# Optimization experiments

Hardware: AMD Instinct MI355X
Metric: run time of the kernel (lower is better)

The kernel has to match this reference:

```python
import jax, jax.numpy as jnp
import numpy as np

BN_EPS = 1e-5

def _mlp(h, w1, b1, w2, b2):
    return jax.nn.relu(h @ w1 + b1) @ w2 + b2

def _segment_mean(data, seg, num_segments):
    s = jax.ops.segment_sum(data, seg, num_segments=num_segments)
    c = jax.ops.segment_sum(jnp.ones((data.shape[0],), data.dtype), seg, num_segments=num_segments)
    return s / jnp.maximum(c, 1.0)[:, None]

def _lin_init(k, fan_in, fan_out):
    k1, k2 = jax.random.split(k)
    s = 1.0 / float(np.sqrt(fan_in))
    w = jax.random.uniform(k1, (fan_in, fan_out), jnp.float32, -s, s)
    b = jax.random.uniform(k2, (fan_out,), jnp.float32, -s, s)
    return w, b

def setup_inputs() -> dict:
    key = jax.random.key(0)
    ks = jax.random.split(key, 16)
    N, E, B = 100000, 1600000, 256
    d1, d2, d3, d5, nc = 3, 50, 15, 10, 6
    x = jax.random.normal(ks[0], (N, d1), jnp.float32)
    edge_index = jax.random.randint(ks[1], (2, E), 0, N)
    edge_attr = jax.random.normal(ks[2], (E, d1), jnp.float32)
    u = jax.random.normal(ks[3], (B, 1), jnp.float32)
    batch = jnp.sort(jax.random.randint(ks[4], (N,), 0, B))
    ew1, eb1 = _lin_init(ks[5], d1 * 3, d2)
    ew2, eb2 = _lin_init(ks[6], d2, d3)
    nw1, nb1 = _lin_init(ks[7], d1 * 6, d2)
    nw2, nb2 = _lin_init(ks[8], d2, d3)
    gw1, gb1 = _lin_init(ks[9], d3 + 1, d2)
    gw2, gb2 = _lin_init(ks[10], d2, d3)
    fc1_w, fc1_b = _lin_init(ks[11], d3, d5)
    bn_g = jnp.ones((d5,), jnp.float32)
    bn_b = jnp.zeros((d5,), jnp.float32)
    fc2_w, fc2_b = _lin_init(ks[12], d5, nc)
    return dict(x=x, edge_index=edge_index, edge_attr=edge_attr, u=u, batch=batch,
                ew1=ew1, eb1=eb1, ew2=ew2, eb2=eb2,
                nw1=nw1, nb1=nb1, nw2=nw2, nb2=nb2,
                gw1=gw1, gb1=gb1, gw2=gw2, gb2=gb2,
                fc1_w=fc1_w, fc1_b=fc1_b, bn_g=bn_g, bn_b=bn_b,
                fc2_w=fc2_w, fc2_b=fc2_b)

def reference(x, edge_index, edge_attr, u, batch,
              ew1, eb1, ew2, eb2, nw1, nb1, nw2, nb2,
              gw1, gb1, gw2, gb2, fc1_w, fc1_b, bn_g, bn_b, fc2_w, fc2_b):
    N = x.shape[0]
    B = u.shape[0]
    row, col = edge_index[0], edge_index[1]
    # edge update: cat([x[row], x[col], edge_attr]) -> MLP  => [E, d3]
    e2 = _mlp(jnp.concatenate([x[row], x[col], edge_attr], axis=1), ew1, eb1, ew2, eb2)
    # node update: cat([x[col], e2]) -> MLP -> scatter_mean over row  => [N, d3]
    h = _mlp(jnp.concatenate([x[col], e2], axis=1), nw1, nb1, nw2, nb2)
    x2 = _segment_mean(h, row, N)
    # global update: cat([u, mean_per_graph(x2)]) -> MLP  => [B, d3]
    u2 = _mlp(jnp.concatenate([u, _segment_mean(x2, batch, B)], axis=1), gw1, gb1, gw2, gb2)
    # readout: relu(cat nodes + globals), mean-pool per graph (u2 rows join their graph)
    z = jax.nn.relu(jnp.concatenate([x2, u2], axis=0))  # dropout off (eval mode)
    seg = jnp.concatenate([batch, jnp.arange(B, dtype=batch.dtype)])
    g = _segment_mean(z, seg, B)  # [B, d3]
    h1 = g @ fc1_w + fc1_b
    # BatchNorm1d in eval mode with default running stats (mean=0, var=1)
    h1 = jax.nn.relu(h1 * (bn_g / jnp.sqrt(1.0 + BN_EPS)) + bn_b)
    return jax.nn.log_softmax(h1 @ fc2_w + fc2_b, axis=1)
```

## Files before the change

### kernel.cpp

```cpp
#include <hip/hip_runtime.h>
#include <math.h>

#define D1 3
#define D2 50
#define D3 15
#define D5 10
#define NC 6
#define SCAN_B 512

typedef _Float16 h2 __attribute__((ext_vector_type(2)));
typedef __fp16   fp16x2 __attribute__((ext_vector_type(2)));

__device__ __forceinline__ float fdot2(h2 a, h2 b, float c) {
#if __has_builtin(__builtin_amdgcn_fdot2)
    return __builtin_amdgcn_fdot2(a, b, c, false);
#else
    return c + (float)a[0] * (float)b[0] + (float)a[1] * (float)b[1];
#endif
}

__device__ __forceinline__ h2 pkrtz(float a, float b) {
#if __has_builtin(__builtin_amdgcn_cvt_pkrtz)
    fp16x2 r = __builtin_amdgcn_cvt_pkrtz(a, b);
    return __builtin_bit_cast(h2, r);
#else
    h2 v; v[0] = (_Float16)a; v[1] = (_Float16)b; return v;
#endif
}

__global__ __launch_bounds__(256) void deg_rank_prep_kernel(
    const int* __restrict__ ei, int* __restrict__ deg, int* __restrict__ rank, int E,
    const float* __restrict__ ew1, const float* __restrict__ nw1,
    const float* __restrict__ ew2, const float* __restrict__ nw2,
    h2* __restrict__ ew1pk, h2* __restrict__ nw1pk,
    h2* __restrict__ ew2pk, h2* __restrict__ nw2pk)
{
    int e = blockIdx.x * blockDim.x + threadIdx.x;
    if (e < E) {
        int r = ei[e];
        rank[e] = atomicAdd(&deg[r], 1);
    }
    if (blockIdx.x == 0) {
        int t = threadIdx.x;
        for (int i = t; i < D2 * 5; i += 256) {
            int j = i / 5, p = i - 5 * j;
            float a = ew1[(2 * p) * D2 + j];
            float b = (2 * p + 1 < 9) ? ew1[(2 * p + 1) * D2 + j] : 0.0f;
            h2 v; v[0] = (_Float16)a; v[1] = (_Float16)b;
            ew1pk[i] = v;
        }
        for (int i = t; i < D2 * 9; i += 256) {
            int j = i / 9, p = i - 9 * j;
            float a = nw1[(2 * p) * D2 + j];
            float b = nw1[(2 * p + 1) * D2 + j];
            h2 v; v[0] = (_Float16)a; v[1] = (_Float16)b;
            nw1pk[i] = v;
        }
        for (int i = t; i < D3 * 25; i += 256) {
            int m = i / 25, k = i - 25 * m;
            float a = ew2[(2 * k) * D3 + m];
            float b = ew2[(2 * k + 1) * D3 + m];
            h2 v; v[0] = (_Float16)a; v[1] = (_Float16)b;
            ew2pk[i] = v;
            float c = nw2[(2 * k) * D3 + m];
            float d = nw2[(2 * k + 1) * D3 + m];
            h2 w; w[0] = (_Float16)c; w[1] = (_Float16)d;
            nw2pk[i] = w;
        }
    }
}

__global__ __launch_bounds__(SCAN_B) void scan1_kernel(
    const int* __restrict__ deg, int* __restrict__ base, int* __restrict__ bsum, int N)
{
    __shared__ int sm[SCAN_B];
    int i = blockIdx.x * SCAN_B + threadIdx.x;
    int v = (i < N) ? deg[i] : 0;
    sm[threadIdx.x] = v;
    __syncthreads();
    #pragma unroll
    for (int s = 1; s < SCAN_B; s <<= 1) {
        int t = (threadIdx.x >= (unsigned)s) ? sm[threadIdx.x - s] : 0;
        __syncthreads();
        sm[threadIdx.x] += t;
        __syncthreads();
    }
    if (i < N) base[i] = sm[threadIdx.x] - v;
    if (threadIdx.x == SCAN_B - 1) bsum[blockIdx.x] = sm[threadIdx.x];
}

__global__ __launch_bounds__(1024) void scan2_kernel(int* __restrict__ bsum, int nb)
{
    __shared__ int sm[1024];
    int v = ((int)threadIdx.x < nb) ? bsum[threadIdx.x] : 0;
    sm[threadIdx.x] = v;
    __syncthreads();
    #pragma unroll
    for (int s = 1; s < 1024; s <<= 1) {
        int t = (threadIdx.x >= (unsigned)s) ? sm[threadIdx.x - s] : 0;
        __syncthreads();
        sm[threadIdx.x] += t;
        __syncthreads();
    }
    if ((int)threadIdx.x < nb) bsum[threadIdx.x] = sm[threadIdx.x] - v;
}

__global__ __launch_bounds__(SCAN_B) void scan3_kernel(
    int* __restrict__ base, const int* __restrict__ bsum, int N)
{
    int i = blockIdx.x * SCAN_B + threadIdx.x;
    if (i < N) base[i] += bsum[blockIdx.x];
}

__global__ __launch_bounds__(256, 4) void edge_mlp_fused_kernel(
    const float* __restrict__ x,
    const int*   __restrict__ ei,
    const float* __restrict__ ea,
    const h2* __restrict__ ew1pk, const float* __restrict__ eb1,
    const h2* __restrict__ ew2pk, const float* __restrict__ eb2,
    const h2* __restrict__ nw1pk, const float* __restrict__ nb1,
    const h2* __restrict__ nw2pk, const float* __restrict__ nb2,
    const int* __restrict__ base, const int* __restrict__ rank,
    unsigned int* __restrict__ hbuf16,
    int E)
{
    int e = blockIdx.x * blockDim.x + threadIdx.x;
    if (e >= E) return;

    int r = ei[e];
    int c = ei[E + e];
    int slot = base[r] + rank[e];

    float in9[9];
    in9[0] = x[3 * r + 0];
    in9[1] = x[3 * r + 1];
    in9[2] = x[3 * r + 2];
    in9[3] = x[3 * c + 0];
    in9[4] = x[3 * c + 1];
    in9[5] = x[3 * c + 2];
    in9[6] = ea[3 * e + 0];
    in9[7] = ea[3 * e + 1];
    in9[8] = ea[3 * e + 2];

    h2 inpk[5];
    inpk[0] = pkrtz(in9[0], in9[1]);
    inpk[1] = pkrtz(in9[2], in9[3]);
    inpk[2] = pkrtz(in9[4], in9[5]);
    inpk[3] = pkrtz(in9[6], in9[7]);
    inpk[4] = pkrtz(in9[8], 0.0f);

    h2 hpk[25];
    #pragma unroll
    for (int jj = 0; jj < 25; ++jj) {
        float a0 = eb1[2 * jj];
        float a1 = eb1[2 * jj + 1];
        #pragma unroll
        for (int p = 0; p < 5; ++p) {
            a0 = fdot2(inpk[p], ew1pk[(2 * jj) * 5 + p], a0);
            a1 = fdot2(inpk[p], ew1pk[(2 * jj + 1) * 5 + p], a1);
        }
        hpk[jj] = pkrtz(fmaxf(a0, 0.0f), fmaxf(a1, 0.0f));
    }

    float e2v[D3];
    #pragma unroll
    for (int m = 0; m < D3; ++m) {
        float a = eb2[m];
        #pragma unroll
        for (int k = 0; k < 25; ++k) a = fdot2(hpk[k], ew2pk[m * 25 + k], a);
        e2v[m] = a;
    }

    h2 vpk[9];
    vpk[0] = pkrtz(in9[3], in9[4]);
    vpk[1] = pkrtz(in9[5], e2v[0]);
    #pragma unroll
    for (int p = 2; p < 9; ++p) vpk[p] = pkrtz(e2v[2 * p - 3], e2v[2 * p - 2]);

    h2 h2pk[25];
    #pragma unroll
    for (int jj = 0; jj < 25; ++jj) {
        float a0 = nb1[2 * jj];
        float a1 = nb1[2 * jj + 1];
        #pragma unroll
        for (int p = 0; p < 9; ++p) {
            a0 = fdot2(vpk[p], nw1pk[(2 * jj) * 9 + p], a0);
            a1 = fdot2(vpk[p], nw1pk[(2 * jj + 1) * 9 + p], a1);
        }
        h2pk[jj] = pkrtz(fmaxf(a0, 0.0f), fmaxf(a1, 0.0f));
    }

    float acc[D3 + 1];
    #pragma unroll
    for (int m = 0; m < D3; ++m) {
        float a = nb2[m];
        #pragma unroll
        for (int k = 0; k < 25; ++k) a = fdot2(h2pk[k], nw2pk[m * 25 + k], a);
        acc[m] = a;
    }
    acc[D3] = 0.0f;

    union { h2 h[8]; uint4 u[2]; } outp;
    #pragma unroll
    for (int p = 0; p < 8; ++p) outp.h[p] = pkrtz(acc[2 * p], acc[2 * p + 1]);

    uint4* dst = (uint4*)(hbuf16 + (size_t)slot * 8);
    dst[0] = outp.u[0];
    dst[1] = outp.u[1];
}

__global__ __launch_bounds__(256) void tail_kernel(
    const unsigned int* __restrict__ hbuf16,
    const int* __restrict__ deg, const int* __restrict__ base,
    const int* __restrict__ batch, int N,
    const float* __restrict__ u,
    const float* __restrict__ gw1, const float* __restrict__ gb1,
    const float* __restrict__ gw2, const float* __restrict__ gb2,
    const float* __restrict__ fc1w, const float* __restrict__ fc1b,
    const float* __restrict__ bng, const float* __restrict__ bnb,
    const float* __restrict__ fc2w, const float* __restrict__ fc2b,
    float* __restrict__ out)
{
    int b = blockIdx.x;
    int tid = threadIdx.x;

    int lo = 0, hi = N;
    while (lo < hi) { int m = (lo + hi) >> 1; if (batch[m] < b) lo = m + 1; else hi = m; }
    int start = lo;
    hi = N;
    while (lo < hi) { int m = (lo + hi) >> 1; if (batch[m] < b + 1) lo = m + 1; else hi = m; }
    int end = lo;

    float sx[D3], sr[D3];
    #pragma unroll
    for (int j = 0; j < D3; ++j) { sx[j] = 0.0f; sr[j] = 0.0f; }

    for (int i = start + tid; i < end; i += 256) {
        int bs = deg ? base[i] : 0;
        int d  = deg[i];
        float acc[16];
        #pragma unroll
        for (int j = 0; j < 16; ++j) acc[j] = 0.0f;
        const uint4* ptr = (const uint4*)(hbuf16 + (size_t)bs * 8);
        for (int k = 0; k < d; ++k) {
            uint4 w0 = ptr[2 * k];
            uint4 w1 = ptr[2 * k + 1];
            unsigned int ws[8] = {w0.x, w0.y, w0.z, w0.w, w1.x, w1.y, w1.z, w1.w};
            #pragma unroll
            for (int p = 0; p < 8; ++p) {
                h2 v = __builtin_bit_cast(h2, ws[p]);
                acc[2 * p]     += (float)v[0];
                acc[2 * p + 1] += (float)v[1];
            }
        }
        float inv = 1.0f / fmaxf((float)d, 1.0f);
        #pragma unroll
        for (int j = 0; j < D3; ++j) {
            float v = acc[j] * inv;
            sx[j] += v;
            sr[j] += fmaxf(v, 0.0f);
        }
    }

    #pragma unroll
    for (int j = 0; j < D3; ++j) {
        #pragma unroll
        for (int s = 32; s > 0; s >>= 1) {
            sx[j] += __shfl_down(sx[j], s);
            sr[j] += __shfl_down(sr[j], s);
        }
    }

    __shared__ float sm[4][2 * D3];
    __shared__ float s_red[2 * D3];
    __shared__ float s_in16[16];
    __shared__ float s_gh[D2];
    __shared__ float s_g[D3];
    __shared__ float s_h1[D5];

    int lane = tid & 63, wid = tid >> 6;
    if (lane == 0) {
        #pragma unroll
        for (int j = 0; j < D3; ++j) { sm[wid][j] = sx[j]; sm[wid][D3 + j] = sr[j]; }
    }
    __syncthreads();

    float nct = (float)(end - start);

    if (tid < 2 * D3) {
        s_red[tid] = sm[0][tid] + sm[1][tid] + sm[2][tid] + sm[3][tid];
    }
    __syncthreads();

    if (tid < 16) {
        s_in16[tid] = (tid == 0) ? u[b] : s_red[tid - 1] / fmaxf(nct, 1.0f);
    }
    __syncthreads();

    if (tid < D2) {
        float a = gb1[tid];
        #pragma unroll
        for (int k = 0; k < 16; ++k) a = fmaf(s_in16[k], gw1[k * D2 + tid], a);
        s_gh[tid] = fmaxf(a, 0.0f);
    }
    __syncthreads();

    if (tid < D3) {
        float a = gb2[tid];
        #pragma unroll
        for (int k = 0; k < D2; ++k) a = fmaf(s_gh[k], gw2[k * D3 + tid], a);
        s_g[tid] = (s_red[D3 + tid] + fmaxf(a, 0.0f)) / (nct + 1.0f);
    }
    __syncthreads();

    if (tid < D5) {
        const float bnscale = 1.0f / sqrtf(1.0f + 1e-5f);
        float a = fc1b[tid];
        #pragma unroll
        for (int k = 0; k < D3; ++k) a = fmaf(s_g[k], fc1w[k * D5 + tid], a);
        s_h1[tid] = fmaxf(a * (bng[tid] * bnscale) + bnb[tid], 0.0f);
    }
    __syncthreads();

    if (tid == 0) {
        float o[NC];
        #pragma unroll
        for (int j = 0; j < NC; ++j) {
            float a = fc2b[j];
            #pragma unroll
            for (int k = 0; k < D5; ++k) a = fmaf(s_h1[k], fc2w[k * NC + j], a);
            o[j] = a;
        }
        float m = o[0];
        #pragma unroll
        for (int j = 1; j < NC; ++j) m = fmaxf(m, o[j]);
        float ssum = 0.0f;
        #pragma unroll
        for (int j = 0; j < NC; ++j) ssum += expf(o[j] - m);
        float lse = m + logf(ssum);
        #pragma unroll
        for (int j = 0; j < NC; ++j) out[b * NC + j] = o[j] - lse;
    }
}

__global__ __launch_bounds__(256) void edge_node_atomic_kernel(
    const float* __restrict__ x,
    const int*   __restrict__ ei,
    const float* __restrict__ ea,
    const float* __restrict__ ew1, const float* __restrict__ eb1,
    const float* __restrict__ ew2, const float* __restrict__ eb2,
    const float* __restrict__ nw1, const float* __restrict__ nb1,
    const float* __restrict__ nw2, const float* __restrict__ nb2,
    float* __restrict__ x2sum, float* __restrict__ cnt,
    int E)
{
    int e = blockIdx.x * blockDim.x + threadIdx.x;
    if (e >= E) return;
    int r = ei[e];
    int c = ei[E + e];
    float in9[9];
    in9[0] = x[3 * r + 0]; in9[1] = x[3 * r + 1]; in9[2] = x[3 * r + 2];
    float xc0 = x[3 * c + 0], xc1 = x[3 * c + 1], xc2 = x[3 * c + 2];
    in9[3] = xc0; in9[4] = xc1; in9[5] = xc2;
    in9[6] = ea[3 * e + 0]; in9[7] = ea[3 * e + 1]; in9[8] = ea[3 * e + 2];
    float h[D2];
    #pragma unroll
    for (int j = 0; j < D2; ++j) {
        float a = eb1[j];
        #pragma unroll
        for (int k = 0; k < 9; ++k) a = fmaf(in9[k], ew1[k * D2 + j], a);
        h[j] = fmaxf(a, 0.0f);
    }
    float e2[D3];
    #pragma unroll
    for (int j = 0; j < D3; ++j) {
        float a = eb2[j];
        #pragma unroll
        for (int k = 0; k < D2; ++k) a = fmaf(h[k], ew2[k * D3 + j], a);
        e2[j] = a;
    }
    float h2v[D2];
    #pragma unroll
    for (int j = 0; j < D2; ++j) {
        float a = nb1[j];
        a = fmaf(xc0, nw1[0 * D2 + j], a);
        a = fmaf(xc1, nw1[1 * D2 + j], a);
        a = fmaf(xc2, nw1[2 * D2 + j], a);
        #pragma unroll
        for (int k = 0; k < D3; ++k) a = fmaf(e2[k], nw1[(3 + k) * D2 + j], a);
        h2v[j] = fmaxf(a, 0.0f);
    }
    float* dst = x2sum + (size_t)r * D3;
    #pragma unroll
    for (int j = 0; j < D3; ++j) {
        float a = nb2[j];
        #pragma unroll
        for (int k = 0; k < D2; ++k) a = fmaf(h2v[k], nw2[k * D3 + j], a);
        atomicAdd(&dst[j], a);
    }
    atomicAdd(&cnt[r], 1.0f);
}

__global__ __launch_bounds__(256) void graph_sum_atomic_kernel(
    const float* __restrict__ x2sum, const float* __restrict__ cnt,
    const int* __restrict__ batch, int N,
    float* __restrict__ bx, float* __restrict__ brelu, float* __restrict__ ncnt)
{
    int b = blockIdx.x;
    int lo = 0, hi = N;
    while (lo < hi) { int m = (lo + hi) >> 1; if (batch[m] < b) lo = m + 1; else hi = m; }
    int start = lo;
    hi = N;
    while (lo < hi) { int m = (lo + hi) >> 1; if (batch[m] < b + 1) lo = m + 1; else hi = m; }
    int end = lo;
    float sx[D3], sr[D3];
    #pragma unroll
    for (int j = 0; j < D3; ++j) { sx[j] = 0.0f; sr[j] = 0.0f; }
    for (int i = start + (int)threadIdx.x; i < end; i += (int)blockDim.x) {
        float inv = 1.0f / fmaxf(cnt[i], 1.0f);
        #pragma unroll
        for (int j = 0; j < D3; ++j) {
            float v = x2sum[(size_t)i * D3 + j] * inv;
            sx[j] += v;
            sr[j] += fmaxf(v, 0.0f);
        }
    }
    #pragma unroll
    for (int j = 0; j < D3; ++j) {
        #pragma unroll
        for (int s = 32; s > 0; s >>= 1) {
            sx[j] += __shfl_down(sx[j], s);
            sr[j] += __shfl_down(sr[j], s);
        }
    }
    __shared__ float sm[4][2 * D3];
    int lane = threadIdx.x & 63, wid = threadIdx.x >> 6;
    if (lane == 0) {
        #pragma unroll
        for (int j = 0; j < D3; ++j) { sm[wid][j] = sx[j]; sm[wid][D3 + j] = sr[j]; }
    }
    __syncthreads();
    if (threadIdx.x < 2 * D3) {
        float v = sm[0][threadIdx.x] + sm[1][threadIdx.x] + sm[2][threadIdx.x] + sm[3][threadIdx.x];
        if (threadIdx.x < D3) bx[b * D3 + threadIdx.x] = v;
        else                  brelu[b * D3 + (threadIdx.x - D3)] = v;
    }
    if (threadIdx.x == 0) ncnt[b] = (float)(end - start);
}

__global__ __launch_bounds__(256) void final_kernel(
    const float* __restrict__ u,
    const float* __restrict__ gw1, const float* __restrict__ gb1,
    const float* __restrict__ gw2, const float* __restrict__ gb2,
    const float* __restrict__ fc1w, const float* __restrict__ fc1b,
    const float* __restrict__ bng, const float* __restrict__ bnb,
    const float* __restrict__ fc2w, const float* __restrict__ fc2b,
    const float* __restrict__ bx, const float* __restrict__ brelu,
    const float* __restrict__ ncnt,
    float* __restrict__ out, int B)
{
    int t = blockIdx.x * blockDim.x + threadIdx.x;
    if (t >= B) return;

    float nct = ncnt[t];
    float inv = 1.0f / fmaxf(nct, 1.0f);

    float in16[16];
    in16[0] = u[t];
    #pragma unroll
    for (int j = 0; j < D3; ++j) in16[1 + j] = bx[t * D3 + j] * inv;

    float gh[D2];
    #pragma unroll
    for (int j = 0; j < D2; ++j) {
        float a = gb1[j];
        #pragma unroll
        for (int k = 0; k < 16; ++k) a = fmaf(in16[k], gw1[k * D2 + j], a);
        gh[j] = fmaxf(a, 0.0f);
    }

    float g[D3];
    #pragma unroll
    for (int j = 0; j < D3; ++j) {
        float a = gb2[j];
        #pragma unroll
        for (int k = 0; k < D2; ++k) a = fmaf(gh[k], gw2[k * D3 + j], a);
        g[j] = (brelu[t * D3 + j] + fmaxf(a, 0.0f)) / (nct + 1.0f);
    }

    const float bnscale = 1.0f / sqrtf(1.0f + 1e-5f);
    float h1[D5];
    #pragma unroll
    for (int i = 0; i < D5; ++i) {
        float a = fc1b[i];
        #pragma unroll
        for (int k = 0; k < D3; ++k) a = fmaf(g[k], fc1w[k * D5 + i], a);
        h1[i] = fmaxf(a * (bng[i] * bnscale) + bnb[i], 0.0f);
    }

    float o[NC];
    #pragma unroll
    for (int j = 0; j < NC; ++j) {
        float a = fc2b[j];
        #pragma unroll
        for (int k = 0; k < D5; ++k) a = fmaf(h1[k], fc2w[k * NC + j], a);
        o[j] = a;
    }
    float m = o[0];
    #pragma unroll
    for (int j = 1; j < NC; ++j) m = fmaxf(m, o[j]);
    float ssum = 0.0f;
    #pragma unroll
    for (int j = 0; j < NC; ++j) ssum += expf(o[j] - m);
    float lse = m + logf(ssum);
    #pragma unroll
    for (int j = 0; j < NC; ++j) out[t * NC + j] = o[j] - lse;
}

extern "C" void kernel_launch(void* const* d_in, const int* in_sizes, int n_in,
                              void* d_out, int out_size, void* d_ws, size_t ws_size,
                              hipStream_t stream) {
    const float* x     = (const float*)d_in[0];
    const int*   ei    = (const int*)  d_in[1];
    const float* ea    = (const float*)d_in[2];
    const float* u     = (const float*)d_in[3];
    const int*   batch = (const int*)  d_in[4];
    const float* ew1 = (const float*)d_in[5];
    const float* eb1 = (const float*)d_in[6];
    const float* ew2 = (const float*)d_in[7];
    const float* eb2 = (const float*)d_in[8];
    const float* nw1 = (const float*)d_in[9];
    const float* nb1 = (const float*)d_in[10];
    const float* nw2 = (const float*)d_in[11];
    const float* nb2 = (const float*)d_in[12];
    const float* gw1 = (const float*)d_in[13];
    const float* gb1 = (const float*)d_in[14];
    const float* gw2 = (const float*)d_in[15];
    const float* gb2 = (const float*)d_in[16];
    const float* fc1w = (const float*)d_in[17];
    const float* fc1b = (const float*)d_in[18];
    const float* bng  = (const float*)d_in[19];
    const float* bnb  = (const float*)d_in[20];
    const float* fc2w = (const float*)d_in[21];
    const float* fc2b = (const float*)d_in[22];

    int N = in_sizes[0] / 3;
    int E = in_sizes[2] / 3;
    int B = in_sizes[3];
    float* out = (float*)d_out;

    int nsb = (N + SCAN_B - 1) / SCAN_B;

    const size_t WPK = 2048;

    size_t need = sizeof(h2) * WPK
                + sizeof(unsigned int) * (size_t)E * 8
                + sizeof(int) * ((size_t)N + (size_t)E + (size_t)N + 1024);

    if (ws_size >= need && nsb <= 1024) {
        char* p = (char*)d_ws;
        h2* ew1pk = (h2*)p;
        h2* nw1pk = ew1pk + 250;
        h2* ew2pk = nw1pk + 450;
        h2* nw2pk = ew2pk + 375;
        p += sizeof(h2) * WPK;
        unsigned int* hbuf16 = (unsigned int*)p;  p += sizeof(unsigned int) * (size_t)E * 8;
        int* deg  = (int*)p;            p += sizeof(int) * (size_t)N;
        int* rank = (int*)p;            p += sizeof(int) * (size_t)E;
        int* base = (int*)p;            p += sizeof(int) * (size_t)N;
        int* bsum = (int*)p;            p += sizeof(int) * 1024;

        hipMemsetAsync(deg, 0, sizeof(int) * (size_t)N, stream);

        int eb = (E + 255) / 256;
        deg_rank_prep_kernel<<<eb, 256, 0, stream>>>(
            ei, deg, rank, E, ew1, nw1, ew2, nw2, ew1pk, nw1pk, ew2pk, nw2pk);

        scan1_kernel<<<nsb, SCAN_B, 0, stream>>>(deg, base, bsum, N);
        scan2_kernel<<<1, 1024, 0, stream>>>(bsum, nsb);
        scan3_kernel<<<nsb, SCAN_B, 0, stream>>>(base, bsum, N);

        edge_mlp_fused_kernel<<<eb, 256, 0, stream>>>(
            x, ei, ea, ew1pk, eb1, ew2pk, eb2, nw1pk, nb1, nw2pk, nb2,
            base, rank, hbuf16, E);

        tail_kernel<<<B, 256, 0, stream>>>(
            hbuf16, deg, base, batch, N,
            u, gw1, gb1, gw2, gb2, fc1w, fc1b, bng, bnb, fc2w, fc2b, out);
    } else {
        float* x2sum = (float*)d_ws;
        float* cnt   = x2sum + (size_t)N * D3;
        float* bx    = cnt + N;
        float* brelu = bx + (size_t)B * D3;
        float* ncnt  = brelu + (size_t)B * D3;

        hipMemsetAsync(x2sum, 0, sizeof(float) * ((size_t)N * D3 + N), stream);

        int eb = (E + 255) / 256;
        edge_node_atomic_kernel<<<eb, 256, 0, stream>>>(
            x, ei, ea, ew1, eb1, ew2, eb2, nw1, nb1, nw2, nb2, x2sum, cnt, E);

        graph_sum_atomic_kernel<<<B, 256, 0, stream>>>(x2sum, cnt, batch, N, bx, brelu, ncnt);

        int fb = (B + 255) / 256;
        final_kernel<<<fb, 256, 0, stream>>>(
            u, gw1, gb1, gw2, gb2, fc1w, fc1b, bng, bnb, fc2w, fc2b,
            bx, brelu, ncnt, out, B);
    }
}
```

Baseline: 209.5 us.

## Parallelize tail reduction across nodes and merge scan passes

Replaces the per-graph tail kernel (256 blocks, one per graph) with a node-parallel partial kernel. Eight threads per node each sum one fp16 pair of that node's segment, then atomically add into shared-memory per-graph accumulators that are flushed to a global gsum buffer. A separate single-thread-per-graph head kernel then runs the small MLP and log-softmax. The second and third scan passes are also fused into one kernel in which each block sums the preceding block totals itself. This targets the low parallelism of the old tail, at the cost of more atomics and redundant bsum reads.

```diff
diff --git a/kernel.cpp b/kernel.cpp
--- a/kernel.cpp
+++ b/kernel.cpp
@@ -7,6 +7,7 @@
 #define D5 10
 #define NC 6
 #define SCAN_B 512
+#define GS 64
 
 typedef _Float16 h2 __attribute__((ext_vector_type(2)));
 typedef __fp16   fp16x2 __attribute__((ext_vector_type(2)));
@@ -89,27 +90,28 @@
     if (threadIdx.x == SCAN_B - 1) bsum[blockIdx.x] = sm[threadIdx.x];
 }
 
-__global__ __launch_bounds__(1024) void scan2_kernel(int* __restrict__ bsum, int nb)
-{
-    __shared__ int sm[1024];
-    int v = ((int)threadIdx.x < nb) ? bsum[threadIdx.x] : 0;
-    sm[threadIdx.x] = v;
+__global__ __launch_bounds__(SCAN_B) void scan23_kernel(
+    int* __restrict__ base, const int* __restrict__ bsum, int N)
+{
+    int bid = blockIdx.x;
+    int sum = 0;
+    for (int t = (int)threadIdx.x; t < bid; t += SCAN_B) sum += bsum[t];
+    #pragma unroll
+    for (int s = 32; s > 0; s >>= 1) sum += __shfl_down(sum, s);
+    __shared__ int ws[SCAN_B / 64];
+    __shared__ int s_total;
+    int lane = threadIdx.x & 63, wid = threadIdx.x >> 6;
+    if (lane == 0) ws[wid] = sum;
     __syncthreads();
-    #pragma unroll
-    for (int s = 1; s < 1024; s <<= 1) {
-        int t = (threadIdx.x >= (unsigned)s) ? sm[threadIdx.x - s] : 0;
-        __syncthreads();
-        sm[threadIdx.x] += t;
-        __syncthreads();
-    }
-    if ((int)threadIdx.x < nb) bsum[threadIdx.x] = sm[threadIdx.x] - v;
-}
-
-__global__ __launch_bounds__(SCAN_B) void scan3_kernel(
-    int* __restrict__ base, const int* __restrict__ bsum, int N)
-{
-    int i = blockIdx.x * SCAN_B + threadIdx.x;
-    if (i < N) base[i] += bsum[blockIdx.x];
+    if (threadIdx.x == 0) {
+        int tot = 0;
+        #pragma unroll
+        for (int w = 0; w < SCAN_B / 64; ++w) tot += ws[w];
+        s_total = tot;
+    }
+    __syncthreads();
+    int i = bid * SCAN_B + threadIdx.x;
+    if (i < N) base[i] += s_total;
 }
 
 __global__ __launch_bounds__(256, 4) void edge_mlp_fused_kernel(
@@ -209,138 +211,132 @@
     dst[1] = outp.u[1];
 }
 
-__global__ __launch_bounds__(256) void tail_kernel(
+__global__ __launch_bounds__(256) void tail_partial_kernel(
     const unsigned int* __restrict__ hbuf16,
     const int* __restrict__ deg, const int* __restrict__ base,
     const int* __restrict__ batch, int N,
+    float* __restrict__ gsum)
+{
+    __shared__ float sacc[16 * GS];
+    int tid = threadIdx.x;
+    #pragma unroll
+    for (int q = tid; q < 16 * GS; q += 256) sacc[q] = 0.0f;
+    __syncthreads();
+
+    int n0 = blockIdx.x * 32;
+    int n  = n0 + (tid >> 3);
+    int p  = tid & 7;
+    int g_first = batch[n0 < N ? n0 : (N - 1)];
+
+    if (n < N) {
+        int bs = base[n];
+        int d  = deg[n];
+        int g  = batch[n];
+        float a0 = 0.0f, a1 = 0.0f;
+        const unsigned int* ptr = hbuf16 + (size_t)bs * 8 + p;
+        for (int k = 0; k < d; ++k) {
+            unsigned int w = ptr[(size_t)k * 8];
+            h2 v = __builtin_bit_cast(h2, w);
+            a0 += (float)v[0];
+            a1 += (float)v[1];
+        }
+        float inv = 1.0f / fmaxf((float)d, 1.0f);
+        float v0 = a0 * inv, v1 = a1 * inv;
+        float r0 = fmaxf(v0, 0.0f), r1 = fmaxf(v1, 0.0f);
+        int sl = g - g_first;
+        if (sl < 16) {
+            atomicAdd(&sacc[sl * GS + 2 * p],          v0);
+            atomicAdd(&sacc[sl * GS + 2 * p + 1],      v1);
+            atomicAdd(&sacc[sl * GS + 32 + 2 * p],     r0);
+            atomicAdd(&sacc[sl * GS + 32 + 2 * p + 1], r1);
+        } else {
+            atomicAdd(&gsum[(size_t)g * GS + 2 * p],          v0);
+            atomicAdd(&gsum[(size_t)g * GS + 2 * p + 1],      v1);
+            atomicAdd(&gsum[(size_t)g * GS + 32 + 2 * p],     r0);
+            atomicAdd(&gsum[(size_t)g * GS + 32 + 2 * p + 1], r1);
+        }
+    }
+    __syncthreads();
+
+    if (tid < GS) {
+        for (int sl = 0; sl < 16; ++sl) {
+            float v = sacc[sl * GS + tid];
+            if (v != 0.0f) atomicAdd(&gsum[(size_t)(g_first + sl) * GS + tid], v);
+        }
+    }
+}
+
+__global__ __launch_bounds__(256) void final_head_kernel(
+    const float* __restrict__ gsum, const int* __restrict__ batch, int N,
     const float* __restrict__ u,
     const float* __restrict__ gw1, const float* __restrict__ gb1,
     const float* __restrict__ gw2, const float* __restrict__ gb2,
     const float* __restrict__ fc1w, const float* __restrict__ fc1b,
     const float* __restrict__ bng, const float* __restrict__ bnb,
     const float* __restrict__ fc2w, const float* __restrict__ fc2b,
-    float* __restrict__ out)
-{
-    int b = blockIdx.x;
-    int tid = threadIdx.x;
+    float* __restrict__ out, int B)
+{
+    int t = blockIdx.x * blockDim.x + threadIdx.x;
+    if (t >= B) return;
 
     int lo = 0, hi = N;
-    while (lo < hi) { int m = (lo + hi) >> 1; if (batch[m] < b) lo = m + 1; else hi = m; }
+    while (lo < hi) { int m = (lo + hi) >> 1; if (batch[m] < t) lo = m + 1; else hi = m; }
     int start = lo;
     hi = N;
-    while (lo < hi) { int m = (lo + hi) >> 1; if (batch[m] < b + 1) lo = m + 1; else hi = m; }
-    int end = lo;
-
-    float sx[D3], sr[D3];
-    #pragma unroll
-    for (int j = 0; j < D3; ++j) { sx[j] = 0.0f; sr[j] = 0.0f; }
-
-    for (int i = start + tid; i < end; i += 256) {
-        int bs = deg ? base[i] : 0;
-        int d  = deg[i];
-        float acc[16];
-        #pragma unroll
-        for (int j = 0; j < 16; ++j) acc[j] = 0.0f;
-        const uint4* ptr = (const uint4*)(hbuf16 + (size_t)bs * 8);
-        for (int k = 0; k < d; ++k) {
-            uint4 w0 = ptr[2 * k];
-            uint4 w1 = ptr[2 * k + 1];
-            unsigned int ws[8] = {w0.x, w0.y, w0.z, w0.w, w1.x, w1.y, w1.z, w1.w};
-            #pragma unroll
-            for (int p = 0; p < 8; ++p) {
-                h2 v = __builtin_bit_cast(h2, ws[p]);
-                acc[2 * p]     += (float)v[0];
-                acc[2 * p + 1] += (float)v[1];
-            }
-        }
-        float inv = 1.0f / fmaxf((float)d, 1.0f);
-        #pragma unroll
-        for (int j = 0; j < D3; ++j) {
-            float v = acc[j] * inv;
-            sx[j] += v;
-            sr[j] += fmaxf(v, 0.0f);
-        }
-    }
-
+    while (lo < hi) { int m = (lo + hi) >> 1; if (batch[m] < t + 1) lo = m + 1; else hi = m; }
+    float nct = (float)(lo - start);
+
+    float in16[16];
+    in16[0] = u[t];
+    float invn = 1.0f / fmaxf(nct, 1.0f);
+    #pragma unroll
+    for (int j = 0; j < D3; ++j) in16[1 + j] = gsum[(size_t)t * GS + j] * invn;
+
+    float gh[D2];
+    #pragma unroll
+    for (int j = 0; j < D2; ++j) {
+        float a = gb1[j];
+        #pragma unroll
+        for (int k = 0; k < 16; ++k) a = fmaf(in16[k], gw1[k * D2 + j], a);
+        gh[j] = fmaxf(a, 0.0f);
+    }
+
+    float g[D3];
     #pragma unroll
     for (int j = 0; j < D3; ++j) {
-        #pragma unroll
-        for (int s = 32; s > 0; s >>= 1) {
-            sx[j] += __shfl_down(sx[j], s);
-            sr[j] += __shfl_down(sr[j], s);
-        }
-    }
-
-    __shared__ float sm[4][2 * D3];
-    __shared__ float s_red[2 * D3];
-    __shared__ float s_in16[16];
-    __shared__ float s_gh[D2];
-    __shared__ float s_g[D3];
-    __shared__ float s_h1[D5];
-
-    int lane = tid & 63, wid = tid >> 6;
-    if (lane == 0) {
-        #pragma unroll
-        for (int j = 0; j < D3; ++j) { sm[wid][j] = sx[j]; sm[wid][D3 + j] = sr[j]; }
-    }
-    __syncthreads();
-
-    float nct = (float)(end - start);
-
-    if (tid < 2 * D3) {
-        s_red[tid] = sm[0][tid] + sm[1][tid] + sm[2][tid] + sm[3][tid];
-    }
-    __syncthreads();
-
-    if (tid < 16) {
-        s_in16[tid] = (tid == 0) ? u[b] : s_red[tid - 1] / fmaxf(nct, 1.0f);
-    }
-    __syncthreads();
-
-    if (tid < D2) {
-        float a = gb1[tid];
-        #pragma unroll
-        for (int k = 0; k < 16; ++k) a = fmaf(s_in16[k], gw1[k * D2 + tid], a);
-        s_gh[tid] = fmaxf(a, 0.0f);
-    }
-    __syncthreads();
-
-    if (tid < D3) {
-        float a = gb2[tid];
-        #pragma unroll
-        for (int k = 0; k < D2; ++k) a = fmaf(s_gh[k], gw2[k * D3 + tid], a);
-        s_g[tid] = (s_red[D3 + tid] + fmaxf(a, 0.0f)) / (nct + 1.0f);
-    }
-    __syncthreads();
-
-    if (tid < D5) {
-        const float bnscale = 1.0f / sqrtf(1.0f + 1e-5f);
-        float a = fc1b[tid];
-        #pragma unroll
-        for (int k = 0; k < D3; ++k) a = fmaf(s_g[k], fc1w[k * D5 + tid], a);
-        s_h1[tid] = fmaxf(a * (bng[tid] * bnscale) + bnb[tid], 0.0f);
-    }
-    __syncthreads();
-
-    if (tid == 0) {
-        float o[NC];
-        #pragma unroll
-        for (int j = 0; j < NC; ++j) {
-            float a = fc2b[j];
-            #pragma unroll
-            for (int k = 0; k < D5; ++k) a = fmaf(s_h1[k], fc2w[k * NC + j], a);
-            o[j] = a;
-        }
-        float m = o[0];
-        #pragma unroll
-        for (int j = 1; j < NC; ++j) m = fmaxf(m, o[j]);
-        float ssum = 0.0f;
-        #pragma unroll
-        for (int j = 0; j < NC; ++j) ssum += expf(o[j] - m);
-        float lse = m + logf(ssum);
-        #pragma unroll
-        for (int j = 0; j < NC; ++j) out[b * NC + j] = o[j] - lse;
-    }
+        float a = gb2[j];
+        #pragma unroll
+        for (int k = 0; k < D2; ++k) a = fmaf(gh[k], gw2[k * D3 + j], a);
+        g[j] = (gsum[(size_t)t * GS + 32 + j] + fmaxf(a, 0.0f)) / (nct + 1.0f);
+    }
+
+    const float bnscale = 1.0f / sqrtf(1.0f + 1e-5f);
+    float h1[D5];
+    #pragma unroll
+    for (int i = 0; i < D5; ++i) {
+        float a = fc1b[i];
+        #pragma unroll
+        for (int k = 0; k < D3; ++k) a = fmaf(g[k], fc1w[k * D5 + i], a);
+        h1[i] = fmaxf(a * (bng[i] * bnscale) + bnb[i], 0.0f);
+    }
+
+    float o[NC];
+    #pragma unroll
+    for (int j = 0; j < NC; ++j) {
+        float a = fc2b[j];
+        #pragma unroll
+        for (int k = 0; k < D5; ++k) a = fmaf(h1[k], fc2w[k * NC + j], a);
+        o[j] = a;
+    }
+    float m = o[0];
+    #pragma unroll
+    for (int j = 1; j < NC; ++j) m = fmaxf(m, o[j]);
+    float ssum = 0.0f;
+    #pragma unroll
+    for (int j = 0; j < NC; ++j) ssum += expf(o[j] - m);
+    float lse = m + logf(ssum);
+    #pragma unroll
+    for (int j = 0; j < NC; ++j) out[t * NC + j] = o[j] - lse;
 }
 
 __global__ __launch_bounds__(256) void edge_node_atomic_kernel(
@@ -461,15 +457,12 @@
 {
     int t = blockIdx.x * blockDim.x + threadIdx.x;
     if (t >= B) return;
-
     float nct = ncnt[t];
     float inv = 1.0f / fmaxf(nct, 1.0f);
-
     float in16[16];
     in16[0] = u[t];
     #pragma unroll
     for (int j = 0; j < D3; ++j) in16[1 + j] = bx[t * D3 + j] * inv;
-
     float gh[D2];
     #pragma unroll
     for (int j = 0; j < D2; ++j) {
@@ -478,7 +471,6 @@
         for (int k = 0; k < 16; ++k) a = fmaf(in16[k], gw1[k * D2 + j], a);
         gh[j] = fmaxf(a, 0.0f);
     }
-
     float g[D3];
     #pragma unroll
     for (int j = 0; j < D3; ++j) {
@@ -487,7 +479,6 @@
         for (int k = 0; k < D2; ++k) a = fmaf(gh[k], gw2[k * D3 + j], a);
         g[j] = (brelu[t * D3 + j] + fmaxf(a, 0.0f)) / (nct + 1.0f);
     }
-
     const float bnscale = 1.0f / sqrtf(1.0f + 1e-5f);
     float h1[D5];
     #pragma unroll
@@ -497,7 +488,6 @@
         for (int k = 0; k < D3; ++k) a = fmaf(g[k], fc1w[k * D5 + i], a);
         h1[i] = fmaxf(a * (bng[i] * bnscale) + bnb[i], 0.0f);
     }
-
     float o[NC];
     #pragma unroll
     for (int j = 0; j < NC; ++j) {
@@ -550,12 +540,13 @@
     float* out = (float*)d_out;
 
     int nsb = (N + SCAN_B - 1) / SCAN_B;
-
     const size_t WPK = 2048;
 
     size_t need = sizeof(h2) * WPK
                 + sizeof(unsigned int) * (size_t)E * 8
-                + sizeof(int) * ((size_t)N + (size_t)E + (size_t)N + 1024);
+                + sizeof(int) * (size_t)N
+                + sizeof(float) * (size_t)B * GS
+                + sizeof(int) * ((size_t)E + (size_t)N + 1024);
 
     if (ws_size >= need && nsb <= 1024) {
         char* p = (char*)d_ws;
@@ -565,28 +556,33 @@
         h2* nw2pk = ew2pk + 375;
         p += sizeof(h2) * WPK;
         unsigned int* hbuf16 = (unsigned int*)p;  p += sizeof(unsigned int) * (size_t)E * 8;
-        int* deg  = (int*)p;            p += sizeof(int) * (size_t)N;
+        int* deg   = (int*)p;           p += sizeof(int) * (size_t)N;
+        float* gsum = (float*)p;        p += sizeof(float) * (size_t)B * GS;
         int* rank = (int*)p;            p += sizeof(int) * (size_t)E;
         int* base = (int*)p;            p += sizeof(int) * (size_t)N;
         int* bsum = (int*)p;            p += sizeof(int) * 1024;
 
-        hipMemsetAsync(deg, 0, sizeof(int) * (size_t)N, stream);
+        hipMemsetAsync(deg, 0, sizeof(int) * (size_t)N + sizeof(float) * (size_t)B * GS, stream);
 
         int eb = (E + 255) / 256;
         deg_rank_prep_kernel<<<eb, 256, 0, stream>>>(
             ei, deg, rank, E, ew1, nw1, ew2, nw2, ew1pk, nw1pk, ew2pk, nw2pk);
 
         scan1_kernel<<<nsb, SCAN_B, 0, stream>>>(deg, base, bsum, N);
-        scan2_kernel<<<1, 1024, 0, stream>>>(bsum, nsb);
-        scan3_kernel<<<nsb, SCAN_B, 0, stream>>>(base, bsum, N);
+        scan23_kernel<<<nsb, SCAN_B, 0, stream>>>(base, bsum, N);
 
         edge_mlp_fused_kernel<<<eb, 256, 0, stream>>>(
             x, ei, ea, ew1pk, eb1, ew2pk, eb2, nw1pk, nb1, nw2pk, nb2,
             base, rank, hbuf16, E);
 
-        tail_kernel<<<B, 256, 0, stream>>>(
-            hbuf16, deg, base, batch, N,
-            u, gw1, gb1, gw2, gb2, fc1w, fc1b, bng, bnb, fc2w, fc2b, out);
+        int ntb = (N + 31) / 32;
+        tail_partial_kernel<<<ntb, 256, 0, stream>>>(
+            hbuf16, deg, base, batch, N, gsum);
+
+        int fb = (B + 255) / 256;
+        final_head_kernel<<<fb, 256, 0, stream>>>(
+            gsum, batch, N, u, gw1, gb1, gw2, gb2,
+            fc1w, fc1b, bng, bnb, fc2w, fc2b, out, B);
     } else {
         float* x2sum = (float*)d_ws;
         float* cnt   = x2sum + (size_t)N * D3;
```

Result: slower. 234.2 us (+11.8%).
